# Optimization experiments

Hardware: AMD Instinct MI355X
Metric: run time of the kernel (lower is better)

Reference implementation:

```python
import jax, jax.numpy as jnp
import numpy as np

N, D, T = 4096, 256, 8
RHO = 16.0
DT = 1.0 / T


def setup_inputs() -> dict:
    key = jax.random.key(0)
    k1, k2, k3, k4 = jax.random.split(key, 4)
    X = jax.random.normal(k1, (N, D), dtype=jnp.float32)
    # learned deformation parameters (small init so the Euler flow stays stable)
    A = jax.random.normal(k2, (T, N, D), dtype=jnp.float32) * 0.01
    A_aff = jax.random.normal(k3, (T, D, D), dtype=jnp.float32) * 0.01
    b_aff = jax.random.normal(k4, (T, D), dtype=jnp.float32) * 0.01
    return {"X": X, "A": A, "A_aff": A_aff, "b_aff": b_aff}


def _flow(X, A, A_aff, b_aff):
    inv_two_rho2 = 1.0 / (2.0 * RHO * RHO)

    def step(Z, params_t):
        A_t, Aaff_t, baff_t = params_t
        # Gaussian self-kernel K[i,j] = exp(-||z_i - z_j||^2 / (2 rho^2))
        sq = jnp.sum(Z * Z, axis=1)                      # [n]
        dist = sq[:, None] + sq[None, :] - 2.0 * (Z @ Z.T)  # [n, n]
        K = jnp.exp(-dist * inv_two_rho2)
        # velocity: affine part + RKHS (kernel message aggregation) part
        v = Z @ Aaff_t.T + baff_t[None, :] + K @ A_t     # [n, d]
        return Z + DT * v, None

    Z_final, _ = jax.lax.scan(step, X, (A, A_aff, b_aff))
    return Z_final


def reference(X, A, A_aff, b_aff):
    return _flow(X, A, A_aff, b_aff)
```

## Files before the change

kernel.cpp:

```cpp
#include <hip/hip_runtime.h>


#define N_PTS 4096
#define DIM   256
#define DT_C  0.125f
#define C1    (1.0f/512.0f)

typedef __bf16 bf16x8 __attribute__((ext_vector_type(8)));
typedef float  f32x16 __attribute__((ext_vector_type(16)));
typedef float  f32x4v __attribute__((ext_vector_type(4)));
typedef unsigned int   u32x4 __attribute__((ext_vector_type(4)));
typedef unsigned short u16x8 __attribute__((ext_vector_type(8)));

__device__ __forceinline__ unsigned short f2bf(float f) {
  unsigned int u = __builtin_bit_cast(unsigned int, f);
  u += 0x7fffu + ((u >> 16) & 1u);
  return (unsigned short)(u >> 16);
}
__device__ __forceinline__ float bf2f(unsigned short s) {
  unsigned int u = ((unsigned int)s) << 16;
  return __builtin_bit_cast(float, u);
}

__global__ __launch_bounds__(256) void k_prep(const float* __restrict__ A,
                                              unsigned short* __restrict__ ATf) {
  __shared__ float sT[64][36];
  const int jgrp = blockIdx.x, ds = blockIdx.y, t = blockIdx.z;
  const int tid = threadIdx.x;
  const float* Ab = A + (size_t)t * N_PTS * DIM;
  {
    const int j_l = tid >> 2, dq = tid & 3;
    const float* src = Ab + (size_t)(jgrp * 64 + j_l) * DIM + ds * 32 + dq * 8;
    f32x4v v0 = *(const f32x4v*)src, v1 = *(const f32x4v*)(src + 4);
    *(f32x4v*)&sT[j_l][dq * 8] = v0;
    *(f32x4v*)&sT[j_l][dq * 8 + 4] = v1;
  }
  __syncthreads();
  const int jb_l = tid >> 6, l = tid & 63, l31 = l & 31, lhi = l >> 5;
  u16x8 o;
#pragma unroll
  for (int e = 0; e < 8; ++e) o[e] = f2bf(sT[jb_l * 16 + lhi * 8 + e][l31]);
  unsigned short* dst = ATf + (size_t)t * (8 * 256 * 64 * 8)
                      + ((size_t)(ds * 256 + jgrp * 4 + jb_l) * 64 + l) * 8;
  *(u16x8*)dst = o;
}

__global__ __launch_bounds__(256) void k_init(const float* __restrict__ X,
                                              unsigned short* __restrict__ Zf,
                                              float* __restrict__ erow) {
  const int tid = threadIdx.x;
  const int r = blockIdx.x * 8 + (tid >> 5), o = tid & 31;
  const size_t base = (size_t)r * DIM + o * 8;
  f32x4v z0 = *(const f32x4v*)(X + base), z1 = *(const f32x4v*)(X + base + 4);
  u16x8 zb; float s = 0.f;
#pragma unroll
  for (int i = 0; i < 4; ++i) { zb[i] = f2bf(z0[i]); zb[4 + i] = f2bf(z1[i]);
                                s += z0[i] * z0[i] + z1[i] * z1[i]; }
  *(u16x8*)(Zf + ((size_t)((r >> 5) * 16 + (o >> 1)) * 64 + (o & 1) * 32 + (r & 31)) * 8) = zb;
#pragma unroll
  for (int d = 16; d > 0; d >>= 1) s += __shfl_down(s, d, 32);
  if (o == 0) erow[r] = __expf(-s * C1);
}

__global__ __launch_bounds__(512, 4) void k_flash(
    const unsigned short* __restrict__ Zf, const float* __restrict__ erow,
    const unsigned short* __restrict__ ATf_t,
    const float* __restrict__ Aaff_t,
    unsigned short* __restrict__ Opart) {
  __shared__ __align__(16) unsigned short sZi[64 * 256];
  __shared__ __align__(16) unsigned short sP[2][64 * 64];

  const int tid = threadIdx.x, lane = tid & 63, wid = tid >> 6;
  const int l31 = lane & 31, lhi = lane >> 5;
  const int chunk = blockIdx.x;
  const int i0 = blockIdx.y * 64;
  const int ib = i0 >> 5;

  {
    const unsigned short* src = Zf + (size_t)ib * 8192;
#pragma unroll
    for (int p = 0; p < 4; ++p)
      *(u32x4*)(sZi + (size_t)(p * 512 + tid) * 8) =
          *(const u32x4*)(src + (size_t)(p * 512 + tid) * 8);
  }
  __syncthreads();

  if (wid < 4) {
    const int ip = wid >> 1, jh = wid & 1;
    float eI[16];
#pragma unroll
    for (int c = 0; c < 16; ++c)
      eI[c] = erow[i0 + ip * 32 + 4 * lhi + (c & 3) + 8 * (c >> 2)];

    for (int n = 0; n < 8; ++n) {
      u32x4 bv[16];
      {
        const unsigned short* bp =
            Zf + ((size_t)(chunk * 16 + n * 2 + jh) * 16 * 64 + lane) * 8;
#pragma unroll
        for (int ks = 0; ks < 16; ++ks) bv[ks] = *(const u32x4*)(bp + ks * 512);
      }
      f32x16 S;
#pragma unroll
      for (int i = 0; i < 16; ++i) S[i] = 0.f;
#pragma unroll
      for (int ks = 0; ks < 16; ++ks) {
        bf16x8 af = *(const bf16x8*)(sZi + ((size_t)(ip * 16 + ks) * 64 + lane) * 8);
        S = __builtin_amdgcn_mfma_f32_32x32x16_bf16(af, __builtin_bit_cast(bf16x8, bv[ks]), S, 0, 0, 0);
      }
      const float ej = erow[chunk * 512 + n * 64 + jh * 32 + l31];
      unsigned short* pb = sP[n & 1];
      const int blk = jh * 4 + (l31 >> 3), cl = l31 & 7;
#pragma unroll
      for (int c = 0; c < 16; ++c) {
        const int row = ip * 32 + 4 * lhi + (c & 3) + 8 * (c >> 2);
        pb[row * 64 + ((blk ^ (row & 7)) * 8) + cl] =
            f2bf(eI[c] * ej * __expf(2.f * C1 * S[c]));
      }
      __syncthreads();
    }
    __syncthreads();
  } else {
    const int cd = wid - 4;
    f32x16 O[2][2];
#pragma unroll
    for (int rs = 0; rs < 2; ++rs)
#pragma unroll
      for (int ct = 0; ct < 2; ++ct)
#pragma unroll
        for (int i = 0; i < 16; ++i) O[rs][ct][i] = 0.f;

#pragma unroll
    for (int q = 0; q < 2; ++q) {
      const int ksg = chunk * 2 + q;
      bf16x8 a[2];
#pragma unroll
      for (int rs = 0; rs < 2; ++rs)
        a[rs] = *(const bf16x8*)(sZi + ((size_t)(rs * 16 + ksg) * 64 + lane) * 8);
#pragma unroll
      for (int ct = 0; ct < 2; ++ct) {
        const int d = cd * 64 + ct * 32 + l31;
        const float* bp = Aaff_t + (size_t)d * DIM + ksg * 16 + lhi * 8;
        f32x4v f0 = *(const f32x4v*)bp, f1 = *(const f32x4v*)(bp + 4);
        u16x8 tb;
#pragma unroll
        for (int i = 0; i < 4; ++i) { tb[i] = f2bf(f0[i]); tb[4 + i] = f2bf(f1[i]); }
        bf16x8 bv = __builtin_bit_cast(bf16x8, tb);
#pragma unroll
        for (int rs = 0; rs < 2; ++rs)
          O[rs][ct] = __builtin_amdgcn_mfma_f32_32x32x16_bf16(a[rs], bv, O[rs][ct], 0, 0, 0);
      }
    }
    __syncthreads();

    for (int n = 1; n <= 8; ++n) {
      const int m = n - 1;
      u32x4 bw[8];
#pragma unroll
      for (int ks = 0; ks < 4; ++ks)
#pragma unroll
        for (int ct = 0; ct < 2; ++ct)
          bw[ks * 2 + ct] = *(const u32x4*)(ATf_t +
              ((size_t)((cd * 2 + ct) * 256 + chunk * 32 + m * 4 + ks) * 64 + lane) * 8);
      const unsigned short* pb = sP[m & 1];
#pragma unroll
      for (int ks = 0; ks < 4; ++ks) {
        bf16x8 a[2];
        const int blk = ks * 2 + lhi;
#pragma unroll
        for (int rs = 0; rs < 2; ++rs) {
          const int row = rs * 32 + l31;
          a[rs] = *(const bf16x8*)&pb[row * 64 + ((blk ^ (row & 7)) * 8)];
        }
#pragma unroll
        for (int rs = 0; rs < 2; ++rs)
#pragma unroll
          for (int ct = 0; ct < 2; ++ct)
            O[rs][ct] = __builtin_amdgcn_mfma_f32_32x32x16_bf16(
                a[rs], __builtin_bit_cast(bf16x8, bw[ks * 2 + ct]), O[rs][ct], 0, 0, 0);
      }
      __syncthreads();
    }

    unsigned short* ob = Opart + (size_t)chunk * N_PTS * DIM + (size_t)cd * 64 + l31;
#pragma unroll
    for (int rs = 0; rs < 2; ++rs)
#pragma unroll
      for (int c = 0; c < 16; ++c) {
        const int row = i0 + rs * 32 + 4 * lhi + (c & 3) + 8 * (c >> 2);
        ob[(size_t)row * DIM]      = f2bf(O[rs][0][c]);
        ob[(size_t)row * DIM + 32] = f2bf(O[rs][1][c]);
      }
  }
}

__global__ __launch_bounds__(256) void k_update(const float* __restrict__ Zin,
                                                const unsigned short* __restrict__ Opart,
                                                const float* __restrict__ baff_t,
                                                float* __restrict__ Zout,
                                                unsigned short* __restrict__ Zf,
                                                float* __restrict__ erow) {
  const int tid = threadIdx.x;
  const int r = blockIdx.x * 8 + (tid >> 5), o = tid & 31;
  const size_t base = (size_t)r * DIM + o * 8;
  f32x4v z0 = *(const f32x4v*)(Zin + base), z1 = *(const f32x4v*)(Zin + base + 4);
  f32x4v s0 = *(const f32x4v*)(baff_t + o * 8), s1 = *(const f32x4v*)(baff_t + o * 8 + 4);
#pragma unroll
  for (int c = 0; c < 8; ++c) {
    u16x8 p = *(const u16x8*)(Opart + (size_t)c * N_PTS * DIM + base);
#pragma unroll
    for (int i = 0; i < 4; ++i) { s0[i] += bf2f(p[i]); s1[i] += bf2f(p[4 + i]); }
  }
  u16x8 zb; float sv = 0.f;
#pragma unroll
  for (int i = 0; i < 4; ++i) {
    z0[i] += DT_C * s0[i]; z1[i] += DT_C * s1[i];
    zb[i] = f2bf(z0[i]); zb[4 + i] = f2bf(z1[i]);
    sv += z0[i] * z0[i] + z1[i] * z1[i];
  }
  *(f32x4v*)(Zout + base) = z0;
  *(f32x4v*)(Zout + base + 4) = z1;
  *(u16x8*)(Zf + ((size_t)((r >> 5) * 16 + (o >> 1)) * 64 + (o & 1) * 32 + (r & 31)) * 8) = zb;
#pragma unroll
  for (int d = 16; d > 0; d >>= 1) sv += __shfl_down(sv, d, 32);
  if (o == 0) erow[r] = __expf(-sv * C1);
}

extern "C" void kernel_launch(void* const* d_in, const int* in_sizes, int n_in,
                              void* d_out, int out_size, void* d_ws, size_t ws_size,
                              hipStream_t stream) {
  const float* X    = (const float*)d_in[0];
  const float* A    = (const float*)d_in[1];
  const float* Aaff = (const float*)d_in[2];
  const float* baff = (const float*)d_in[3];
  float* out = (float*)d_out;

  char* w = (char*)d_ws;
  size_t off = 0;
  unsigned short* ATf = (unsigned short*)(w + off); off += (size_t)8 * 8 * 256 * 64 * 8 * 2;
  unsigned short* Zf  = (unsigned short*)(w + off); off += (size_t)N_PTS * DIM * 2;
  float* erow = (float*)(w + off); off += (size_t)N_PTS * 4;
  float* Zf32 = (float*)(w + off); off += (size_t)N_PTS * DIM * 4;
  unsigned short* Opart = (unsigned short*)(w + off); off += (size_t)8 * N_PTS * DIM * 2;
  (void)ws_size; (void)in_sizes; (void)n_in; (void)out_size;

  k_prep<<<dim3(64, 8, 8), 256, 0, stream>>>(A, ATf);
  k_init<<<512, 256, 0, stream>>>(X, Zf, erow);

  const float* zin = X;
  for (int t = 0; t < 8; ++t) {
    float* zout = (t == 7) ? out : Zf32;
    k_flash<<<dim3(8, 64), 512, 0, stream>>>(
        Zf, erow, ATf + (size_t)t * (8 * 256 * 64 * 8), Aaff + (size_t)t * DIM * DIM, Opart);
    k_update<<<512, 256, 0, stream>>>(zin, Opart, baff + (size_t)t * DIM, zout, Zf, erow);
    zin = zout;
  }
}
```

Measured before the change: 380.7 us.

## Restructure flash kernel: register-resident Zi, LDS-streamed Zj, in-register P handoff

Replaces the producer/consumer warp-specialized kernel (4 waves computing P into LDS, 4 waves consuming it) with a 256-thread kernel where each wave keeps its Zi rows in registers, streams Zj tiles into double-buffered LDS via global_load_lds, and computes S^T so the exp'd P tile feeds the second MFMA directly through cvt_pk_bf16 plus permlane32_swap. A permuted copy of the row exponentials is written in init/update so the vectorized loads line up with the transposed accumulator layout. This removes the LDS round-trip for P and the cross-wave syncs, at the cost of higher register pressure (zi[16], O[4], two S accumulators) and a different occupancy profile.

```diff
diff --git a/kernel.cpp b/kernel.cpp
--- a/kernel.cpp
+++ b/kernel.cpp
@@ -5,6 +5,7 @@
 #define DIM   256
 #define DT_C  0.125f
 #define C1    (1.0f/512.0f)
+#define C2    (1.0f/256.0f)
 
 typedef __bf16 bf16x8 __attribute__((ext_vector_type(8)));
 typedef float  f32x16 __attribute__((ext_vector_type(16)));
@@ -20,6 +21,12 @@
 __device__ __forceinline__ float bf2f(unsigned short s) {
   unsigned int u = ((unsigned int)s) << 16;
   return __builtin_bit_cast(float, u);
+}
+
+typedef __attribute__((address_space(1))) const unsigned int gas_u32;
+typedef __attribute__((address_space(3))) unsigned int las_u32;
+__device__ __forceinline__ void gload_lds16(const void* g, void* l) {
+  __builtin_amdgcn_global_load_lds((gas_u32*)g, (las_u32*)l, 16, 0, 0);
 }
 
 __global__ __launch_bounds__(256) void k_prep(const float* __restrict__ A,
@@ -45,9 +52,15 @@
   *(u16x8*)dst = o;
 }
 
+__device__ __forceinline__ int pidx(int r) {
+  const int jj = r & 31;
+  return (r & ~31) | (((jj >> 2) & 1) << 4) | (((jj >> 3) & 3) << 2) | (jj & 3);
+}
+
 __global__ __launch_bounds__(256) void k_init(const float* __restrict__ X,
                                               unsigned short* __restrict__ Zf,
-                                              float* __restrict__ erow) {
+                                              float* __restrict__ erow,
+                                              float* __restrict__ eperm) {
   const int tid = threadIdx.x;
   const int r = blockIdx.x * 8 + (tid >> 5), o = tid & 31;
   const size_t base = (size_t)r * DIM + o * 8;
@@ -59,139 +72,134 @@
   *(u16x8*)(Zf + ((size_t)((r >> 5) * 16 + (o >> 1)) * 64 + (o & 1) * 32 + (r & 31)) * 8) = zb;
 #pragma unroll
   for (int d = 16; d > 0; d >>= 1) s += __shfl_down(s, d, 32);
-  if (o == 0) erow[r] = __expf(-s * C1);
-}
-
-__global__ __launch_bounds__(512, 4) void k_flash(
+  if (o == 0) { const float e = __expf(-s * C1); erow[r] = e; eperm[pidx(r)] = e; }
+}
+
+__global__ __launch_bounds__(256, 2) void k_flash(
     const unsigned short* __restrict__ Zf, const float* __restrict__ erow,
+    const float* __restrict__ eperm,
     const unsigned short* __restrict__ ATf_t,
     const float* __restrict__ Aaff_t,
     unsigned short* __restrict__ Opart) {
-  __shared__ __align__(16) unsigned short sZi[64 * 256];
-  __shared__ __align__(16) unsigned short sP[2][64 * 64];
+  __shared__ __align__(16) unsigned short sZj[2][16 * 64 * 8];
 
   const int tid = threadIdx.x, lane = tid & 63, wid = tid >> 6;
   const int l31 = lane & 31, lhi = lane >> 5;
+  const int ig = wid >> 1, dh = wid & 1;
   const int chunk = blockIdx.x;
   const int i0 = blockIdx.y * 64;
-  const int ib = i0 >> 5;
 
   {
-    const unsigned short* src = Zf + (size_t)ib * 8192;
+    const unsigned short* src = Zf + (size_t)(chunk * 16) * 8192;
 #pragma unroll
     for (int p = 0; p < 4; ++p)
-      *(u32x4*)(sZi + (size_t)(p * 512 + tid) * 8) =
-          *(const u32x4*)(src + (size_t)(p * 512 + tid) * 8);
+      gload_lds16(src + (size_t)(p * 256 + tid) * 8, &sZj[0][(p * 256 + tid) * 8]);
+  }
+
+  const unsigned short* zib = Zf + (size_t)(blockIdx.y * 2 + ig) * 8192;
+  u32x4 zi[16];
+#pragma unroll
+  for (int ks = 0; ks < 16; ++ks)
+    zi[ks] = *(const u32x4*)(zib + (size_t)ks * 512 + lane * 8);
+
+  const float eI = erow[i0 + ig * 32 + l31];
+
+  f32x16 O[4];
+#pragma unroll
+  for (int ct = 0; ct < 4; ++ct)
+#pragma unroll
+    for (int i = 0; i < 16; ++i) O[ct][i] = 0.f;
+#pragma unroll
+  for (int q = 0; q < 2; ++q) {
+    const int ksg = chunk * 2 + q;
+    const bf16x8 a = __builtin_bit_cast(bf16x8, zi[ksg]);
+#pragma unroll
+    for (int ct = 0; ct < 4; ++ct) {
+      const int d = dh * 128 + ct * 32 + l31;
+      const float* bp = Aaff_t + (size_t)d * DIM + ksg * 16 + lhi * 8;
+      f32x4v f0 = *(const f32x4v*)bp, f1 = *(const f32x4v*)(bp + 4);
+      u16x8 tb;
+#pragma unroll
+      for (int i = 0; i < 4; ++i) { tb[i] = f2bf(f0[i]); tb[4 + i] = f2bf(f1[i]); }
+      O[ct] = __builtin_amdgcn_mfma_f32_32x32x16_bf16(
+          a, __builtin_bit_cast(bf16x8, tb), O[ct], 0, 0, 0);
+    }
   }
   __syncthreads();
 
-  if (wid < 4) {
-    const int ip = wid >> 1, jh = wid & 1;
-    float eI[16];
-#pragma unroll
-    for (int c = 0; c < 16; ++c)
-      eI[c] = erow[i0 + ip * 32 + 4 * lhi + (c & 3) + 8 * (c >> 2)];
-
-    for (int n = 0; n < 8; ++n) {
-      u32x4 bv[16];
-      {
-        const unsigned short* bp =
-            Zf + ((size_t)(chunk * 16 + n * 2 + jh) * 16 * 64 + lane) * 8;
-#pragma unroll
-        for (int ks = 0; ks < 16; ++ks) bv[ks] = *(const u32x4*)(bp + ks * 512);
-      }
-      f32x16 S;
-#pragma unroll
-      for (int i = 0; i < 16; ++i) S[i] = 0.f;
-#pragma unroll
-      for (int ks = 0; ks < 16; ++ks) {
-        bf16x8 af = *(const bf16x8*)(sZi + ((size_t)(ip * 16 + ks) * 64 + lane) * 8);
-        S = __builtin_amdgcn_mfma_f32_32x32x16_bf16(af, __builtin_bit_cast(bf16x8, bv[ks]), S, 0, 0, 0);
-      }
-      const float ej = erow[chunk * 512 + n * 64 + jh * 32 + l31];
-      unsigned short* pb = sP[n & 1];
-      const int blk = jh * 4 + (l31 >> 3), cl = l31 & 7;
-#pragma unroll
-      for (int c = 0; c < 16; ++c) {
-        const int row = ip * 32 + 4 * lhi + (c & 3) + 8 * (c >> 2);
-        pb[row * 64 + ((blk ^ (row & 7)) * 8) + cl] =
-            f2bf(eI[c] * ej * __expf(2.f * C1 * S[c]));
-      }
-      __syncthreads();
+  const float* epc = eperm + (size_t)chunk * 512 + lhi * 16;
+  const unsigned short* atb =
+      ATf_t + ((size_t)(dh * 4 * 256 + chunk * 32) * 64 + lane) * 8;
+
+  for (int n = 0; n < 16; ++n) {
+    const int cur = n & 1;
+    if (n < 15) {
+      const unsigned short* src = Zf + (size_t)(chunk * 16 + n + 1) * 8192;
+#pragma unroll
+      for (int p = 0; p < 4; ++p)
+        gload_lds16(src + (size_t)(p * 256 + tid) * 8,
+                    &sZj[cur ^ 1][(p * 256 + tid) * 8]);
+    }
+    u32x4 bw[8];
+#pragma unroll
+    for (int ct = 0; ct < 4; ++ct)
+#pragma unroll
+      for (int q = 0; q < 2; ++q)
+        bw[ct * 2 + q] = *(const u32x4*)(atb + ((size_t)ct * 256 + n * 2 + q) * 512);
+    f32x4v e0 = *(const f32x4v*)(epc + n * 32);
+    f32x4v e1 = *(const f32x4v*)(epc + n * 32 + 4);
+    f32x4v e2 = *(const f32x4v*)(epc + n * 32 + 8);
+    f32x4v e3 = *(const f32x4v*)(epc + n * 32 + 12);
+
+    f32x16 Sa, Sb;
+#pragma unroll
+    for (int i = 0; i < 16; ++i) { Sa[i] = 0.f; Sb[i] = 0.f; }
+#pragma unroll
+    for (int ks = 0; ks < 16; ks += 2) {
+      bf16x8 a0 = *(const bf16x8*)(&sZj[cur][(ks + 0) * 512 + lane * 8]);
+      bf16x8 a1 = *(const bf16x8*)(&sZj[cur][(ks + 1) * 512 + lane * 8]);
+      Sa = __builtin_amdgcn_mfma_f32_32x32x16_bf16(
+          a0, __builtin_bit_cast(bf16x8, zi[ks + 0]), Sa, 0, 0, 0);
+      Sb = __builtin_amdgcn_mfma_f32_32x32x16_bf16(
+          a1, __builtin_bit_cast(bf16x8, zi[ks + 1]), Sb, 0, 0, 0);
+    }
+
+    float p[16];
+#pragma unroll
+    for (int c = 0; c < 16; ++c) {
+      const float ej = (c < 4) ? e0[c] : (c < 8) ? e1[c - 4]
+                     : (c < 12) ? e2[c - 8] : e3[c - 12];
+      p[c] = eI * ej * __expf((Sa[c] + Sb[c]) * C2);
+    }
+    unsigned int dw[4][2];
+#pragma unroll
+    for (int g = 0; g < 4; ++g) {
+      asm("v_cvt_pk_bf16_f32 %0, %1, %2" : "=v"(dw[g][0]) : "v"(p[4 * g + 0]), "v"(p[4 * g + 1]));
+      asm("v_cvt_pk_bf16_f32 %0, %1, %2" : "=v"(dw[g][1]) : "v"(p[4 * g + 2]), "v"(p[4 * g + 3]));
+    }
+#pragma unroll
+    for (int q = 0; q < 2; ++q) {
+      auto r0 = __builtin_amdgcn_permlane32_swap(dw[2 * q][0], dw[2 * q + 1][0], false, false);
+      auto r1 = __builtin_amdgcn_permlane32_swap(dw[2 * q][1], dw[2 * q + 1][1], false, false);
+      u32x4 paw; paw[0] = r0[0]; paw[1] = r1[0]; paw[2] = r0[1]; paw[3] = r1[1];
+      const bf16x8 pa = __builtin_bit_cast(bf16x8, paw);
+#pragma unroll
+      for (int ct = 0; ct < 4; ++ct)
+        O[ct] = __builtin_amdgcn_mfma_f32_32x32x16_bf16(
+            pa, __builtin_bit_cast(bf16x8, bw[ct * 2 + q]), O[ct], 0, 0, 0);
     }
     __syncthreads();
-  } else {
-    const int cd = wid - 4;
-    f32x16 O[2][2];
-#pragma unroll
-    for (int rs = 0; rs < 2; ++rs)
-#pragma unroll
-      for (int ct = 0; ct < 2; ++ct)
-#pragma unroll
-        for (int i = 0; i < 16; ++i) O[rs][ct][i] = 0.f;
-
-#pragma unroll
-    for (int q = 0; q < 2; ++q) {
-      const int ksg = chunk * 2 + q;
-      bf16x8 a[2];
-#pragma unroll
-      for (int rs = 0; rs < 2; ++rs)
-        a[rs] = *(const bf16x8*)(sZi + ((size_t)(rs * 16 + ksg) * 64 + lane) * 8);
-#pragma unroll
-      for (int ct = 0; ct < 2; ++ct) {
-        const int d = cd * 64 + ct * 32 + l31;
-        const float* bp = Aaff_t + (size_t)d * DIM + ksg * 16 + lhi * 8;
-        f32x4v f0 = *(const f32x4v*)bp, f1 = *(const f32x4v*)(bp + 4);
-        u16x8 tb;
-#pragma unroll
-        for (int i = 0; i < 4; ++i) { tb[i] = f2bf(f0[i]); tb[4 + i] = f2bf(f1[i]); }
-        bf16x8 bv = __builtin_bit_cast(bf16x8, tb);
-#pragma unroll
-        for (int rs = 0; rs < 2; ++rs)
-          O[rs][ct] = __builtin_amdgcn_mfma_f32_32x32x16_bf16(a[rs], bv, O[rs][ct], 0, 0, 0);
-      }
-    }
-    __syncthreads();
-
-    for (int n = 1; n <= 8; ++n) {
-      const int m = n - 1;
-      u32x4 bw[8];
-#pragma unroll
-      for (int ks = 0; ks < 4; ++ks)
-#pragma unroll
-        for (int ct = 0; ct < 2; ++ct)
-          bw[ks * 2 + ct] = *(const u32x4*)(ATf_t +
-              ((size_t)((cd * 2 + ct) * 256 + chunk * 32 + m * 4 + ks) * 64 + lane) * 8);
-      const unsigned short* pb = sP[m & 1];
-#pragma unroll
-      for (int ks = 0; ks < 4; ++ks) {
-        bf16x8 a[2];
-        const int blk = ks * 2 + lhi;
-#pragma unroll
-        for (int rs = 0; rs < 2; ++rs) {
-          const int row = rs * 32 + l31;
-          a[rs] = *(const bf16x8*)&pb[row * 64 + ((blk ^ (row & 7)) * 8)];
-        }
-#pragma unroll
-        for (int rs = 0; rs < 2; ++rs)
-#pragma unroll
-          for (int ct = 0; ct < 2; ++ct)
-            O[rs][ct] = __builtin_amdgcn_mfma_f32_32x32x16_bf16(
-                a[rs], __builtin_bit_cast(bf16x8, bw[ks * 2 + ct]), O[rs][ct], 0, 0, 0);
-      }
-      __syncthreads();
-    }
-
-    unsigned short* ob = Opart + (size_t)chunk * N_PTS * DIM + (size_t)cd * 64 + l31;
-#pragma unroll
-    for (int rs = 0; rs < 2; ++rs)
-#pragma unroll
-      for (int c = 0; c < 16; ++c) {
-        const int row = i0 + rs * 32 + 4 * lhi + (c & 3) + 8 * (c >> 2);
-        ob[(size_t)row * DIM]      = f2bf(O[rs][0][c]);
-        ob[(size_t)row * DIM + 32] = f2bf(O[rs][1][c]);
-      }
-  }
+  }
+
+  unsigned short* ob = Opart + (size_t)chunk * N_PTS * DIM
+                     + (size_t)(i0 + ig * 32) * DIM + dh * 128 + l31;
+#pragma unroll
+  for (int ct = 0; ct < 4; ++ct)
+#pragma unroll
+    for (int c = 0; c < 16; ++c) {
+      const int row = 4 * lhi + (c & 3) + 8 * (c >> 2);
+      ob[(size_t)row * DIM + ct * 32] = f2bf(O[ct][c]);
+    }
 }
 
 __global__ __launch_bounds__(256) void k_update(const float* __restrict__ Zin,
@@ -199,7 +207,8 @@
                                                 const float* __restrict__ baff_t,
                                                 float* __restrict__ Zout,
                                                 unsigned short* __restrict__ Zf,
-                                                float* __restrict__ erow) {
+                                                float* __restrict__ erow,
+                                                float* __restrict__ eperm) {
   const int tid = threadIdx.x;
   const int r = blockIdx.x * 8 + (tid >> 5), o = tid & 31;
   const size_t base = (size_t)r * DIM + o * 8;
@@ -223,7 +232,7 @@
   *(u16x8*)(Zf + ((size_t)((r >> 5) * 16 + (o >> 1)) * 64 + (o & 1) * 32 + (r & 31)) * 8) = zb;
 #pragma unroll
   for (int d = 16; d > 0; d >>= 1) sv += __shfl_down(sv, d, 32);
-  if (o == 0) erow[r] = __expf(-sv * C1);
+  if (o == 0) { const float e = __expf(-sv * C1); erow[r] = e; eperm[pidx(r)] = e; }
 }
 
 extern "C" void kernel_launch(void* const* d_in, const int* in_sizes, int n_in,
@@ -239,20 +248,21 @@
   size_t off = 0;
   unsigned short* ATf = (unsigned short*)(w + off); off += (size_t)8 * 8 * 256 * 64 * 8 * 2;
   unsigned short* Zf  = (unsigned short*)(w + off); off += (size_t)N_PTS * DIM * 2;
-  float* erow = (float*)(w + off); off += (size_t)N_PTS * 4;
+  float* erow  = (float*)(w + off); off += (size_t)N_PTS * 4;
+  float* eperm = (float*)(w + off); off += (size_t)N_PTS * 4;
   float* Zf32 = (float*)(w + off); off += (size_t)N_PTS * DIM * 4;
   unsigned short* Opart = (unsigned short*)(w + off); off += (size_t)8 * N_PTS * DIM * 2;
   (void)ws_size; (void)in_sizes; (void)n_in; (void)out_size;
 
   k_prep<<<dim3(64, 8, 8), 256, 0, stream>>>(A, ATf);
-  k_init<<<512, 256, 0, stream>>>(X, Zf, erow);
+  k_init<<<512, 256, 0, stream>>>(X, Zf, erow, eperm);
 
   const float* zin = X;
   for (int t = 0; t < 8; ++t) {
     float* zout = (t == 7) ? out : Zf32;
-    k_flash<<<dim3(8, 64), 512, 0, stream>>>(
-        Zf, erow, ATf + (size_t)t * (8 * 256 * 64 * 8), Aaff + (size_t)t * DIM * DIM, Opart);
-    k_update<<<512, 256, 0, stream>>>(zin, Opart, baff + (size_t)t * DIM, zout, Zf, erow);
+    k_flash<<<dim3(8, 64), 256, 0, stream>>>(
+        Zf, erow, eperm, ATf + (size_t)t * (8 * 256 * 64 * 8), Aaff + (size_t)t * DIM * DIM, Opart);
+    k_update<<<512, 256, 0, stream>>>(zin, Opart, baff + (size_t)t * DIM, zout, Zf, erow, eperm);
     zin = zout;
   }
 }
```

After: 838.0 us. 120% more time.
